# Optimization experiments

Measured on AMD Instinct MI355X. Metric: run time of the kernel, lower is better.

## Reference

```python
import jax, jax.numpy as jnp
import numpy as np

N_VERTS = 163842  # icosphere level-7 mesh
C = 128
K = 7  # vertex + 6 one-ring neighbors
BN_EPS = 1e-5


def setup_inputs() -> dict:
    key = jax.random.key(0)
    ks = jax.random.split(key, 4)
    x = jax.random.normal(ks[0], (N_VERTS, C), dtype=jnp.float32)
    neigh_orders = jax.random.randint(ks[1], (N_VERTS * K,), 0, N_VERTS, dtype=jnp.int64)
    W1 = jax.random.normal(ks[2], (C, K * C), dtype=jnp.float32) * 0.02
    b1 = jnp.zeros((C,), dtype=jnp.float32)
    gamma1 = jnp.ones((C,), dtype=jnp.float32)
    beta1 = jnp.zeros((C,), dtype=jnp.float32)
    W2 = jax.random.normal(ks[3], (C, K * C), dtype=jnp.float32) * 0.02
    b2 = jnp.zeros((C,), dtype=jnp.float32)
    gamma2 = jnp.ones((C,), dtype=jnp.float32)
    beta2 = jnp.zeros((C,), dtype=jnp.float32)
    return {"x": x, "neigh_orders": neigh_orders, "W1": W1, "b1": b1,
            "gamma1": gamma1, "beta1": beta1, "W2": W2, "b2": b2,
            "gamma2": gamma2, "beta2": beta2}


def _onering_conv(x, neigh_orders, W, b):
    # gather [N*7, C] -> [N, 7*C], then linear
    feat = x[neigh_orders].reshape(x.shape[0], -1)
    return feat @ W.T + b


def _batchnorm(h, gamma, beta):
    # training-mode BatchNorm1d over the vertex (batch) dim, biased variance
    mean = jnp.mean(h, axis=0)
    var = jnp.var(h, axis=0)
    return (h - mean) * jax.lax.rsqrt(var + BN_EPS) * gamma + beta


def _leaky_relu(h):
    return jnp.where(h >= 0, h, 0.2 * h)


def reference(x, neigh_orders, W1, b1, gamma1, beta1, W2, b2, gamma2, beta2):
    h = _onering_conv(x, neigh_orders, W1, b1)
    h = _leaky_relu(_batchnorm(h, gamma1, beta1))
    h = _onering_conv(h, neigh_orders, W2, b2)
    h = _batchnorm(h, gamma2, beta2)
    return _leaky_relu(h + x)  # first_in_block=False -> plain residual
```

## Files before the change

### kernel.cpp

```cpp
#include <hip/hip_runtime.h>

#define NV 163842
#define NC 128
#define KN 7
#define NWELT (NC * KN * NC)
#define BN_EPS 1e-5f
#define NBLK 1281
#define RG 32
#define RROWS 41

typedef __attribute__((ext_vector_type(4))) float f32x4;
typedef __attribute__((ext_vector_type(8))) short bf16x8;
typedef __attribute__((ext_vector_type(8))) unsigned short u16x8;

static __device__ __forceinline__ unsigned short f2bf(float f) {
    union { float f; unsigned int u; } v; v.f = f;
    unsigned int r = v.u + 0x7fffu + ((v.u >> 16) & 1u);
    return (unsigned short)(r >> 16);
}
static __device__ __forceinline__ float bf2f(unsigned short s) {
    union { unsigned int u; float f; } v; v.u = ((unsigned int)s) << 16;
    return v.f;
}
static __device__ __forceinline__ void gload_lds16(const void* g, void* l) {
    __builtin_amdgcn_global_load_lds((const __attribute__((address_space(1))) void*)g,
                                     (__attribute__((address_space(3))) void*)l, 16, 0, 0);
}

__global__ void cvt_kernel(const float* __restrict__ x, const float* __restrict__ w1,
                           const float* __restrict__ w2, unsigned short* __restrict__ xbf,
                           unsigned short* __restrict__ w1bf, unsigned short* __restrict__ w2bf)
{
    const int total4 = (NV * NC + 2 * NWELT) / 4;
    for (int i = blockIdx.x * blockDim.x + threadIdx.x; i < total4; i += gridDim.x * blockDim.x) {
        int e = i * 4;
        const float* src; unsigned short* dst;
        if (e < NV * NC)              { src = x  + e;                  dst = xbf  + e; }
        else if (e < NV * NC + NWELT) { src = w1 + (e - NV * NC);      dst = w1bf + (e - NV * NC); }
        else                          { src = w2 + (e - NV * NC - NWELT); dst = w2bf + (e - NV * NC - NWELT); }
        float4 v = *(const float4*)src;
        ushort4 o;
        o.x = f2bf(v.x); o.y = f2bf(v.y); o.z = f2bf(v.z); o.w = f2bf(v.w);
        *(ushort4*)dst = o;
    }
}

__global__ __launch_bounds__(512, 2)
void conv_kernel(const unsigned short* __restrict__ xin,
                 const int* __restrict__ neigh,
                 const unsigned short* __restrict__ wbf,
                 unsigned short* __restrict__ hout,
                 float* __restrict__ psum, float* __restrict__ psq)
{
    __shared__ __align__(16) char smem[131072];

    const int t    = threadIdx.x;
    const int row0 = blockIdx.x * 128;
    const int w    = t >> 6;
    const int lane = t & 63;
    const int lrow = lane & 15;
    const int lgrp = lane >> 4;
    const int wr   = w >> 2;
    const int wc   = w & 3;

    const int sl   = lane & 7;
    const int r3   = lane >> 3;
    const int srcoff = (sl ^ r3) << 4;

    const int rA0 = w * 16 + r3;
    const int g0  = (row0 + rA0     < NV) ? (row0 + rA0)     : (NV - 1);
    const int g1  = (row0 + rA0 + 8 < NV) ? (row0 + rA0 + 8) : (NV - 1);

    int idx0[KN], idx1[KN];
    #pragma unroll
    for (int k = 0; k < KN; ++k) {
        idx0[k] = neigh[g0 * KN + k];
        idx1[k] = neigh[g1 * KN + k];
    }

    const char* xinb = (const char*)xin;
    const char* bsrc0 = (const char*)wbf + (size_t)(w * 16 + r3) * 1792 + srcoff;
    const char* bsrc1 = (const char*)wbf + (size_t)(w * 16 + 8 + r3) * 1792 + srcoff;

    f32x4 acc[4][2];
    #pragma unroll
    for (int mf = 0; mf < 4; ++mf)
        #pragma unroll
        for (int nf = 0; nf < 2; ++nf)
            acc[mf][nf] = (f32x4){0.f, 0.f, 0.f, 0.f};

#define STAGE(c) do {                                                                 \
        const int k_ = (c) >> 1, h_ = (c) & 1;                                        \
        char* lA = smem + ((c) & 3) * 32768 + w * 2048;                               \
        char* lB = lA + 16384;                                                        \
        gload_lds16(xinb + (size_t)idx0[k_] * 256 + h_ * 128 + srcoff, lA);           \
        gload_lds16(xinb + (size_t)idx1[k_] * 256 + h_ * 128 + srcoff, lA + 1024);    \
        gload_lds16(bsrc0 + k_ * 256 + h_ * 128, lB);                                 \
        gload_lds16(bsrc1 + k_ * 256 + h_ * 128, lB + 1024);                          \
    } while (0)

    STAGE(0); STAGE(1); STAGE(2);
    asm volatile("s_waitcnt vmcnt(8)" ::: "memory");
    __builtin_amdgcn_sched_barrier(0);
    __builtin_amdgcn_s_barrier();
    __builtin_amdgcn_sched_barrier(0);

    #pragma unroll
    for (int c = 0; c < 14; ++c) {
        if (c < 11) STAGE(c + 3);
        __builtin_amdgcn_sched_barrier(0);

        const char* Ab = smem + (c & 3) * 32768;
        const char* Bb = Ab + 16384;
        #pragma unroll
        for (int ks = 0; ks < 2; ++ks) {
            const int koff = ks * 64 + lgrp * 16;
            bf16x8 a[4], b[2];
            #pragma unroll
            for (int mf = 0; mf < 4; ++mf) {
                const int arow = wr * 64 + mf * 16 + lrow;
                a[mf] = *(const bf16x8*)(Ab + ((arow * 128 + koff) ^ ((arow & 7) << 4)));
            }
            #pragma unroll
            for (int nf = 0; nf < 2; ++nf) {
                const int bcol = wc * 32 + nf * 16 + lrow;
                b[nf] = *(const bf16x8*)(Bb + ((bcol * 128 + koff) ^ ((bcol & 7) << 4)));
            }
            #pragma unroll
            for (int mf = 0; mf < 4; ++mf) {
                acc[mf][0] = __builtin_amdgcn_mfma_f32_16x16x32_bf16(a[mf], b[0], acc[mf][0], 0, 0, 0);
                acc[mf][1] = __builtin_amdgcn_mfma_f32_16x16x32_bf16(a[mf], b[1], acc[mf][1], 0, 0, 0);
            }
        }

        if (c < 13) {
            __builtin_amdgcn_sched_barrier(0);
            if (c <= 10)      asm volatile("s_waitcnt vmcnt(8)" ::: "memory");
            else if (c == 11) asm volatile("s_waitcnt vmcnt(4)" ::: "memory");
            else              asm volatile("s_waitcnt vmcnt(0)" ::: "memory");
            __builtin_amdgcn_sched_barrier(0);
            __builtin_amdgcn_s_barrier();
            __builtin_amdgcn_sched_barrier(0);
        }
    }
#undef STAGE

    float* redsum = (float*)smem;
    float* redsq  = (float*)(smem + 1024);

    #pragma unroll
    for (int nf = 0; nf < 2; ++nf) {
        const int col = wc * 32 + nf * 16 + lrow;
        float sum = 0.f, sq = 0.f;
        #pragma unroll
        for (int mf = 0; mf < 4; ++mf) {
            const int rbase = row0 + wr * 64 + mf * 16 + lgrp * 4;
            #pragma unroll
            for (int r = 0; r < 4; ++r) {
                float v = acc[mf][nf][r];
                const int grow = rbase + r;
                if (grow < NV) {
                    sum += v; sq += v * v;
                    hout[(size_t)grow * NC + col] = f2bf(v);
                }
            }
        }
        sum += __shfl_xor(sum, 16); sum += __shfl_xor(sum, 32);
        sq  += __shfl_xor(sq, 16);  sq  += __shfl_xor(sq, 32);
        if (lgrp == 0) { redsum[wr * 128 + col] = sum; redsq[wr * 128 + col] = sq; }
    }
    __syncthreads();
    if (t < 128) {
        psum[(size_t)blockIdx.x * 128 + t] = redsum[t] + redsum[128 + t];
        psq[(size_t)blockIdx.x * 128 + t]  = redsq[t]  + redsq[128 + t];
    }
}

__global__ void bn_reduce_kernel(const float* __restrict__ psum, const float* __restrict__ psq,
                                 float* __restrict__ psum2, float* __restrict__ psq2)
{
    const int c = threadIdx.x;
    const int g = blockIdx.x;
    const int b0 = g * RROWS;
    const int b1 = (b0 + RROWS < NBLK) ? b0 + RROWS : NBLK;
    float s = 0.f, q = 0.f;
    for (int b = b0; b < b1; ++b) {
        s += psum[b * 128 + c];
        q += psq[b * 128 + c];
    }
    psum2[g * 128 + c] = s;
    psq2[g * 128 + c]  = q;
}

__global__ void bn_finalize_kernel(const float* __restrict__ psum2, const float* __restrict__ psq2,
                                   const float* __restrict__ gamma, const float* __restrict__ beta,
                                   float* __restrict__ scale, float* __restrict__ shift)
{
    const int c = threadIdx.x;
    float s = 0.f, q = 0.f;
    #pragma unroll
    for (int g = 0; g < RG; ++g) { s += psum2[g * 128 + c]; q += psq2[g * 128 + c]; }
    const float inv  = 1.f / (float)NV;
    const float mean = s * inv;
    const float var  = q * inv - mean * mean;
    const float sc   = gamma[c] * rsqrtf(var + BN_EPS);
    scale[c] = sc;
    shift[c] = beta[c] - mean * sc;
}

__global__ void bn_apply_kernel(const unsigned short* __restrict__ h, const float* __restrict__ scale,
                                const float* __restrict__ shift, unsigned short* __restrict__ outbf)
{
    __shared__ float ssc[NC], ssh[NC];
    if (threadIdx.x < NC) { ssc[threadIdx.x] = scale[threadIdx.x]; ssh[threadIdx.x] = shift[threadIdx.x]; }
    __syncthreads();
    const int total8 = NV * NC / 8;
    for (int i = blockIdx.x * blockDim.x + threadIdx.x; i < total8; i += gridDim.x * blockDim.x) {
        const int e = i * 8;
        const int c0 = e & (NC - 1);
        u16x8 v = *(const u16x8*)(h + e);
        u16x8 o;
        #pragma unroll
        for (int j = 0; j < 8; ++j) {
            float a = bf2f(v[j]) * ssc[c0 + j] + ssh[c0 + j];
            a = a >= 0.f ? a : 0.2f * a;
            o[j] = f2bf(a);
        }
        *(u16x8*)(outbf + e) = o;
    }
}

__global__ void final_kernel(const unsigned short* __restrict__ h, const float* __restrict__ x,
                             const unsigned short* __restrict__ xb, const int use_bf,
                             const float* __restrict__ scale, const float* __restrict__ shift,
                             float* __restrict__ out)
{
    __shared__ float ssc[NC], ssh[NC];
    if (threadIdx.x < NC) { ssc[threadIdx.x] = scale[threadIdx.x]; ssh[threadIdx.x] = shift[threadIdx.x]; }
    __syncthreads();
    const int total8 = NV * NC / 8;
    for (int i = blockIdx.x * blockDim.x + threadIdx.x; i < total8; i += gridDim.x * blockDim.x) {
        const int e = i * 8;
        const int c0 = e & (NC - 1);
        u16x8 v = *(const u16x8*)(h + e);
        float xv[8];
        if (use_bf) {
            u16x8 xvb = *(const u16x8*)(xb + e);
            #pragma unroll
            for (int j = 0; j < 8; ++j) xv[j] = bf2f(xvb[j]);
        } else {
            float4 x0 = *(const float4*)(x + e);
            float4 x1 = *(const float4*)(x + e + 4);
            xv[0]=x0.x; xv[1]=x0.y; xv[2]=x0.z; xv[3]=x0.w;
            xv[4]=x1.x; xv[5]=x1.y; xv[6]=x1.z; xv[7]=x1.w;
        }
        float ov[8];
        #pragma unroll
        for (int j = 0; j < 8; ++j) {
            float a = bf2f(v[j]) * ssc[c0 + j] + ssh[c0 + j] + xv[j];
            ov[j] = a >= 0.f ? a : 0.2f * a;
        }
        float4 o0 = {ov[0], ov[1], ov[2], ov[3]};
        float4 o1 = {ov[4], ov[5], ov[6], ov[7]};
        *(float4*)(out + e)     = o0;
        *(float4*)(out + e + 4) = o1;
    }
}

extern "C" void kernel_launch(void* const* d_in, const int* in_sizes, int n_in,
                              void* d_out, int out_size, void* d_ws, size_t ws_size,
                              hipStream_t stream)
{
    const float* x      = (const float*)d_in[0];
    const int*   neigh  = (const int*)d_in[1];
    const float* W1     = (const float*)d_in[2];
    const float* gamma1 = (const float*)d_in[4];
    const float* beta1  = (const float*)d_in[5];
    const float* W2     = (const float*)d_in[6];
    const float* gamma2 = (const float*)d_in[8];
    const float* beta2  = (const float*)d_in[9];

    unsigned short* h1pre = (unsigned short*)d_out;
    unsigned short* h1bn  = (unsigned short*)d_out + (size_t)NV * NC;
    float* out = (float*)d_out;

    char* ws = (char*)d_ws;
    size_t off = 0;
    unsigned short* xbf  = (unsigned short*)(ws + off); off += (size_t)NV * NC * 2;
    unsigned short* w1bf = (unsigned short*)(ws + off); off += NWELT * 2;
    unsigned short* w2bf = (unsigned short*)(ws + off); off += NWELT * 2;
    float* psum  = (float*)(ws + off); off += (size_t)NBLK * 128 * 4;
    float* psq   = (float*)(ws + off); off += (size_t)NBLK * 128 * 4;
    float* psum2 = (float*)(ws + off); off += RG * 128 * 4;
    float* psq2  = (float*)(ws + off); off += RG * 128 * 4;
    float* scale1 = (float*)(ws + off); off += 512;
    float* shift1 = (float*)(ws + off); off += 512;
    float* scale2 = (float*)(ws + off); off += 512;
    float* shift2 = (float*)(ws + off); off += 512;

    const size_t h2_bytes = (size_t)NV * NC * 2;
    unsigned short* h2pre;
    int use_bf;
    if (off + h2_bytes <= ws_size) { h2pre = (unsigned short*)(ws + off); use_bf = 1; }
    else                           { h2pre = xbf;                        use_bf = 0; }

    cvt_kernel<<<2048, 256, 0, stream>>>(x, W1, W2, xbf, w1bf, w2bf);
    conv_kernel<<<NBLK, 512, 0, stream>>>(xbf, neigh, w1bf, h1pre, psum, psq);
    bn_reduce_kernel<<<RG, 128, 0, stream>>>(psum, psq, psum2, psq2);
    bn_finalize_kernel<<<1, 128, 0, stream>>>(psum2, psq2, gamma1, beta1, scale1, shift1);
    bn_apply_kernel<<<2048, 256, 0, stream>>>(h1pre, scale1, shift1, h1bn);
    conv_kernel<<<NBLK, 512, 0, stream>>>(h1bn, neigh, w2bf, h2pre, psum, psq);
    bn_reduce_kernel<<<RG, 128, 0, stream>>>(psum, psq, psum2, psq2);
    bn_finalize_kernel<<<1, 128, 0, stream>>>(psum2, psq2, gamma2, beta2, scale2, shift2);
    final_kernel<<<2048, 256, 0, stream>>>(h2pre, x, xbf, use_bf, scale2, shift2, out);
}
```

Before: 222.2 us.

## Halve conv LDS pipeline depth for occupancy and merge BN reduction kernels

The conv kernel goes from a 4-stage to a 2-stage (double-buffered) LDS pipeline. This halves shared memory to 64 KB so two blocks can fit per CU, and launch bounds are raised accordingly. Each stage now waits for all outstanding loads, which trades prefetch depth for occupancy. Separately, the two BN reduce/finalize kernels are replaced by one per-channel kernel that reduces with wave shuffles, removing a launch and an intermediate buffer.

```diff
diff --git a/kernel.cpp b/kernel.cpp
--- a/kernel.cpp
+++ b/kernel.cpp
@@ -6,8 +6,6 @@
 #define NWELT (NC * KN * NC)
 #define BN_EPS 1e-5f
 #define NBLK 1281
-#define RG 32
-#define RROWS 41
 
 typedef __attribute__((ext_vector_type(4))) float f32x4;
 typedef __attribute__((ext_vector_type(8))) short bf16x8;
@@ -45,14 +43,14 @@
     }
 }
 
-__global__ __launch_bounds__(512, 2)
+__global__ __launch_bounds__(512, 4)
 void conv_kernel(const unsigned short* __restrict__ xin,
                  const int* __restrict__ neigh,
                  const unsigned short* __restrict__ wbf,
                  unsigned short* __restrict__ hout,
                  float* __restrict__ psum, float* __restrict__ psq)
 {
-    __shared__ __align__(16) char smem[131072];
+    __shared__ __align__(16) char smem[65536];
 
     const int t    = threadIdx.x;
     const int row0 = blockIdx.x * 128;
@@ -89,28 +87,26 @@
         for (int nf = 0; nf < 2; ++nf)
             acc[mf][nf] = (f32x4){0.f, 0.f, 0.f, 0.f};
 
-#define STAGE(c) do {                                                                 \
-        const int k_ = (c) >> 1, h_ = (c) & 1;                                        \
-        char* lA = smem + ((c) & 3) * 32768 + w * 2048;                               \
-        char* lB = lA + 16384;                                                        \
-        gload_lds16(xinb + (size_t)idx0[k_] * 256 + h_ * 128 + srcoff, lA);           \
-        gload_lds16(xinb + (size_t)idx1[k_] * 256 + h_ * 128 + srcoff, lA + 1024);    \
-        gload_lds16(bsrc0 + k_ * 256 + h_ * 128, lB);                                 \
-        gload_lds16(bsrc1 + k_ * 256 + h_ * 128, lB + 1024);                          \
+#define STAGE(c) do {                                                              \
+        const int h_ = (c) & 1, k_ = (c) >> 1, bs_ = ((c) & 1) * 32768;            \
+        char* lA = smem + bs_ + w * 2048;                                          \
+        char* lB = smem + bs_ + 16384 + w * 2048;                                  \
+        gload_lds16(xinb + (size_t)idx0[k_] * 256 + h_ * 128 + srcoff, lA);        \
+        gload_lds16(xinb + (size_t)idx1[k_] * 256 + h_ * 128 + srcoff, lA + 1024); \
+        gload_lds16(bsrc0 + k_ * 256 + h_ * 128, lB);                              \
+        gload_lds16(bsrc1 + k_ * 256 + h_ * 128, lB + 1024);                       \
     } while (0)
 
-    STAGE(0); STAGE(1); STAGE(2);
-    asm volatile("s_waitcnt vmcnt(8)" ::: "memory");
-    __builtin_amdgcn_sched_barrier(0);
+    STAGE(0);
+    asm volatile("s_waitcnt vmcnt(0)" ::: "memory");
     __builtin_amdgcn_s_barrier();
     __builtin_amdgcn_sched_barrier(0);
 
     #pragma unroll
     for (int c = 0; c < 14; ++c) {
-        if (c < 11) STAGE(c + 3);
-        __builtin_amdgcn_sched_barrier(0);
-
-        const char* Ab = smem + (c & 3) * 32768;
+        if (c < 13) STAGE(c + 1);
+
+        const char* Ab = smem + (c & 1) * 32768;
         const char* Bb = Ab + 16384;
         #pragma unroll
         for (int ks = 0; ks < 2; ++ks) {
@@ -134,10 +130,7 @@
         }
 
         if (c < 13) {
-            __builtin_amdgcn_sched_barrier(0);
-            if (c <= 10)      asm volatile("s_waitcnt vmcnt(8)" ::: "memory");
-            else if (c == 11) asm volatile("s_waitcnt vmcnt(4)" ::: "memory");
-            else              asm volatile("s_waitcnt vmcnt(0)" ::: "memory");
+            asm volatile("s_waitcnt vmcnt(0)" ::: "memory");
             __builtin_amdgcn_sched_barrier(0);
             __builtin_amdgcn_s_barrier();
             __builtin_amdgcn_sched_barrier(0);
@@ -176,36 +169,35 @@
     }
 }
 
-__global__ void bn_reduce_kernel(const float* __restrict__ psum, const float* __restrict__ psq,
-                                 float* __restrict__ psum2, float* __restrict__ psq2)
-{
-    const int c = threadIdx.x;
-    const int g = blockIdx.x;
-    const int b0 = g * RROWS;
-    const int b1 = (b0 + RROWS < NBLK) ? b0 + RROWS : NBLK;
+__global__ void bn_stats_kernel(const float* __restrict__ psum, const float* __restrict__ psq,
+                                const float* __restrict__ gamma, const float* __restrict__ beta,
+                                float* __restrict__ scale, float* __restrict__ shift)
+{
+    const int c = blockIdx.x;
+    const int t = threadIdx.x;
     float s = 0.f, q = 0.f;
-    for (int b = b0; b < b1; ++b) {
+    for (int b = t; b < NBLK; b += 128) {
         s += psum[b * 128 + c];
         q += psq[b * 128 + c];
     }
-    psum2[g * 128 + c] = s;
-    psq2[g * 128 + c]  = q;
-}
-
-__global__ void bn_finalize_kernel(const float* __restrict__ psum2, const float* __restrict__ psq2,
-                                   const float* __restrict__ gamma, const float* __restrict__ beta,
-                                   float* __restrict__ scale, float* __restrict__ shift)
-{
-    const int c = threadIdx.x;
-    float s = 0.f, q = 0.f;
-    #pragma unroll
-    for (int g = 0; g < RG; ++g) { s += psum2[g * 128 + c]; q += psq2[g * 128 + c]; }
-    const float inv  = 1.f / (float)NV;
-    const float mean = s * inv;
-    const float var  = q * inv - mean * mean;
-    const float sc   = gamma[c] * rsqrtf(var + BN_EPS);
-    scale[c] = sc;
-    shift[c] = beta[c] - mean * sc;
+    #pragma unroll
+    for (int o = 1; o < 64; o <<= 1) {
+        s += __shfl_xor(s, o);
+        q += __shfl_xor(q, o);
+    }
+    __shared__ float ls[2], lq[2];
+    if ((t & 63) == 0) { ls[t >> 6] = s; lq[t >> 6] = q; }
+    __syncthreads();
+    if (t == 0) {
+        const float S = ls[0] + ls[1];
+        const float Q = lq[0] + lq[1];
+        const float inv  = 1.f / (float)NV;
+        const float mean = S * inv;
+        const float var  = Q * inv - mean * mean;
+        const float sc   = gamma[c] * rsqrtf(var + BN_EPS);
+        scale[c] = sc;
+        shift[c] = beta[c] - mean * sc;
+    }
 }
 
 __global__ void bn_apply_kernel(const unsigned short* __restrict__ h, const float* __restrict__ scale,
@@ -291,8 +283,6 @@
     unsigned short* w2bf = (unsigned short*)(ws + off); off += NWELT * 2;
     float* psum  = (float*)(ws + off); off += (size_t)NBLK * 128 * 4;
     float* psq   = (float*)(ws + off); off += (size_t)NBLK * 128 * 4;
-    float* psum2 = (float*)(ws + off); off += RG * 128 * 4;
-    float* psq2  = (float*)(ws + off); off += RG * 128 * 4;
     float* scale1 = (float*)(ws + off); off += 512;
     float* shift1 = (float*)(ws + off); off += 512;
     float* scale2 = (float*)(ws + off); off += 512;
@@ -306,11 +296,9 @@
 
     cvt_kernel<<<2048, 256, 0, stream>>>(x, W1, W2, xbf, w1bf, w2bf);
     conv_kernel<<<NBLK, 512, 0, stream>>>(xbf, neigh, w1bf, h1pre, psum, psq);
-    bn_reduce_kernel<<<RG, 128, 0, stream>>>(psum, psq, psum2, psq2);
-    bn_finalize_kernel<<<1, 128, 0, stream>>>(psum2, psq2, gamma1, beta1, scale1, shift1);
+    bn_stats_kernel<<<128, 128, 0, stream>>>(psum, psq, gamma1, beta1, scale1, shift1);
     bn_apply_kernel<<<2048, 256, 0, stream>>>(h1pre, scale1, shift1, h1bn);
     conv_kernel<<<NBLK, 512, 0, stream>>>(h1bn, neigh, w2bf, h2pre, psum, psq);
-    bn_reduce_kernel<<<RG, 128, 0, stream>>>(psum, psq, psum2, psq2);
-    bn_finalize_kernel<<<1, 128, 0, stream>>>(psum2, psq2, gamma2, beta2, scale2, shift2);
+    bn_stats_kernel<<<128, 128, 0, stream>>>(psum, psq, gamma2, beta2, scale2, shift2);
     final_kernel<<<2048, 256, 0, stream>>>(h2pre, x, xbf, use_bf, scale2, shift2, out);
 }
```

Result: faster. 187.1 us (-15.8%).
